# Performance work log

Hardware: AMD Instinct MI355X
Metric: run time of the kernel (lower is better)

Reference implementation:

```python
import jax, jax.numpy as jnp
import numpy as np

DIM = 640
HEADS = 8
SEG = DIM // 5                  # 128 per-segment channels
CH = (DIM // 5 * 4) // HEADS    # 64 per-head dim of the attention branch
SCALE = (DIM // HEADS) ** -0.5  # head_dim in __init__ uses full dim
EPS = 1e-5


def hardswish(x):
    return x * jnp.clip(x + 3.0, 0.0, 6.0) * (1.0 / 6.0)


def dwconv(x, w, pad):
    # x: (B,C,H,W), w: (C,kh,kw) depthwise kernel
    c = x.shape[1]
    return jax.lax.conv_general_dilated(
        x, w[:, None], (1, 1), [(pad, pad), (pad, pad)],
        feature_group_count=c, dimension_numbers=('NCHW', 'OIHW', 'NCHW'))


def pconv(x, w):
    # 1x1 pointwise conv, w: (out,in)
    return jnp.einsum('bchw,oc->bohw', x, w)


def bneval(x, g, b):
    # eval-mode BatchNorm2d with running_mean=0, running_var=1
    s = g * (1.0 / jnp.sqrt(1.0 + EPS))
    return x * s[None, :, None, None] + b[None, :, None, None]


def layernorm(x, g, b):
    m = x.mean(-1, keepdims=True)
    v = x.var(-1, keepdims=True)
    return (x - m) / jnp.sqrt(v + EPS) * g + b


def aggregator(x, Hs, Ws, dw3, dw5, dw7, pw, ln_g, ln_b, bn_g, bn_b):
    # x: (B_,N,C) -> heads tensor (B_,h,N,Ch) for 4 attention segments + local Agg_0 branch (B_,N,SEG)
    B_, N, C = x.shape
    xi = x.transpose(0, 2, 1).reshape(B_, C, Hs, Ws)
    segs = [xi[:, i * SEG:(i + 1) * SEG] for i in range(5)]
    # Agg_0: sepconv3x3 -> LayerNorm(channel-last) -> hardswish
    loc = pconv(dwconv(segs[4], dw3[0], 1), pw[0])
    loc = hardswish(layernorm(loc.reshape(B_, SEG, N).transpose(0, 2, 1), ln_g, ln_b))
    x0 = hardswish(bneval(segs[0], bn_g[0], bn_b[0]))
    x1 = hardswish(bneval(pconv(dwconv(segs[1], dw3[1], 1), pw[1]), bn_g[1], bn_b[1]))
    x2 = hardswish(bneval(pconv(dwconv(segs[2], dw5, 2), pw[2]), bn_g[2], bn_b[2]))
    x3 = hardswish(bneval(pconv(dwconv(segs[3], dw7, 3), pw[3]), bn_g[3], bn_b[3]))
    xt = jnp.concatenate([x0, x1, x2, x3], axis=1)           # (B_, 4*SEG, H, W)
    xt = xt.reshape(B_, HEADS, CH, N).transpose(0, 1, 3, 2)  # (B_, h, N, Ch)
    return xt, loc


def conv_rel_pos_enc(q, v, Hs, Ws, w3, w5, w7):
    # grouped depthwise convs over v image, head splits {3:2,5:3,7:3}
    B, h, N, Ch = q.shape
    v_img = v.transpose(0, 1, 3, 2).reshape(B, h * Ch, Hs, Ws)
    s1, s2 = 2 * Ch, 5 * Ch
    c = jnp.concatenate([dwconv(v_img[:, :s1], w3, 1),
                         dwconv(v_img[:, s1:s2], w5, 2),
                         dwconv(v_img[:, s2:], w7, 3)], axis=1)
    c = c.reshape(B, h, Ch, N).transpose(0, 1, 3, 2)
    return q * c


def _forward(x, y, kv_w, proj_w, proj_b, crpe_w3, crpe_w5, crpe_w7,
             aq_dw3, aq_dw5, aq_dw7, aq_pw, aq_ln_g, aq_ln_b, aq_bn_g, aq_bn_b,
             akv_dw3, akv_dw5, akv_dw7, akv_pw, akv_ln_g, akv_ln_b, akv_bn_g, akv_bn_b,
             Hs, Ws):
    B = x.shape[0]
    N = Hs * Ws
    kv = jnp.einsum('bhwc,oc->bhwo', x, kv_w).reshape(B, Hs, Ws, 2, DIM)
    kv = kv.transpose(3, 0, 1, 2, 4).reshape(2 * B, N, DIM)
    q = y.reshape(B, N, DIM)
    kvh, kv_loc = aggregator(kv, Hs, Ws, akv_dw3, akv_dw5, akv_dw7, akv_pw,
                             akv_ln_g, akv_ln_b, akv_bn_g, akv_bn_b)
    qh, q_loc = aggregator(q, Hs, Ws, aq_dw3, aq_dw5, aq_dw7, aq_pw,
                           aq_ln_g, aq_ln_b, aq_bn_g, aq_bn_b)
    kvh = kvh.reshape(2, B, HEADS, N, CH)
    k, v = kvh[0], kvh[1]
    kv_loc = kv_loc.reshape(2, B, N, SEG)[1]  # local features from the v branch
    k_sm = jax.nn.softmax(k, axis=2)                        # softmax over tokens
    kTv = jnp.einsum('bhnk,bhnv->bhkv', k_sm, v)            # (B,h,Ch,Ch)
    eff = jnp.einsum('bhnk,bhkv->bhnv', qh, kTv)            # (B,h,N,Ch)
    cr = conv_rel_pos_enc(qh, v, Hs, Ws, crpe_w3, crpe_w5, crpe_w7)
    o = SCALE * eff + cr
    o = o.transpose(0, 2, 1, 3).reshape(B, N, HEADS * CH)   # (B,N,4*SEG)
    o = jnp.concatenate([o, kv_loc + q_loc], axis=-1)       # (B,N,DIM)
    return jnp.einsum('bnc,oc->bno', o, proj_w) + proj_b


def setup_inputs():
    ks = jax.random.split(jax.random.key(0), 24)
    def n(i, shape, s=1.0):
        return jax.random.normal(ks[i], shape, dtype=jnp.float32) * s
    inp = {
        'x': n(0, (8, 64, 64, 640)), 'y': n(1, (8, 64, 64, 640)),
        'kv_w': n(2, (1280, 640), 0.02), 'proj_w': n(3, (640, 640), 0.02), 'proj_b': n(4, (640,), 0.02),
        'crpe_w3': n(5, (128, 3, 3), 0.1), 'crpe_w5': n(6, (192, 5, 5), 0.05), 'crpe_w7': n(7, (192, 7, 7), 0.03),
        'aq_dw3': n(8, (2, 128, 3, 3), 0.1), 'aq_dw5': n(9, (128, 5, 5), 0.05), 'aq_dw7': n(10, (128, 7, 7), 0.03),
        'aq_pw': n(11, (4, 128, 128), 0.05),
        'aq_ln_g': 1.0 + n(12, (128,), 0.1), 'aq_ln_b': n(13, (128,), 0.1),
        'aq_bn_g': 1.0 + n(14, (4, 128), 0.1), 'aq_bn_b': n(15, (4, 128), 0.1),
        'akv_dw3': n(16, (2, 128, 3, 3), 0.1), 'akv_dw5': n(17, (128, 5, 5), 0.05), 'akv_dw7': n(18, (128, 7, 7), 0.03),
        'akv_pw': n(19, (4, 128, 128), 0.05),
        'akv_ln_g': 1.0 + n(20, (128,), 0.1), 'akv_ln_b': n(21, (128,), 0.1),
        'akv_bn_g': 1.0 + n(22, (4, 128), 0.1), 'akv_bn_b': n(23, (4, 128), 0.1),
        'H': 64, 'W': 64,
    }
    return inp


def reference(x, y, kv_w, proj_w, proj_b, crpe_w3, crpe_w5, crpe_w7,
              aq_dw3, aq_dw5, aq_dw7, aq_pw, aq_ln_g, aq_ln_b, aq_bn_g, aq_bn_b,
              akv_dw3, akv_dw5, akv_dw7, akv_pw, akv_ln_g, akv_ln_b, akv_bn_g, akv_bn_b,
              H, W):
    return _forward(x, y, kv_w, proj_w, proj_b, crpe_w3, crpe_w5, crpe_w7,
                    aq_dw3, aq_dw5, aq_dw7, aq_pw, aq_ln_g, aq_ln_b, aq_bn_g, aq_bn_b,
                    akv_dw3, akv_dw5, akv_dw7, akv_pw, akv_ln_g, akv_ln_b, akv_bn_g, akv_bn_b,
                    H, W)
```

## Files before the change

### kernel.cpp

```cpp
#include <hip/hip_runtime.h>
#include <hip/hip_bf16.h>
#include <stdint.h>

#define BATCH 8
#define NTOK 4096
#define DIM 640
#define SEG 128
#define NHEADS 8
#define CH 64
#define SCALE_F 0.11180339887498948f
#define EPS_F 1e-5f
#define BNSCALE 0.99999500003749972f

typedef unsigned short u16;
typedef float f32x4 __attribute__((ext_vector_type(4)));
typedef short bf16x8 __attribute__((ext_vector_type(8)));

__device__ __forceinline__ float b2f(u16 u){
  union { float f; unsigned int i; } c; c.i = ((unsigned int)u)<<16; return c.f;
}
__device__ __forceinline__ u16 f2b(float f){
  union { float f; unsigned int i; } c; c.f = f;
  unsigned int i = c.i;
  return (u16)((i + 0x7fffu + ((i>>16)&1u)) >> 16);
}
__device__ __forceinline__ float hswish(float v){
  return v * fminf(fmaxf(v+3.f,0.f),6.f) * (1.f/6.f);
}

__global__ void cvt_k(const float* __restrict__ in, u16* __restrict__ out, int n){
  int idx = (blockIdx.x*256 + threadIdx.x)*4;
  if (idx>=n) return;
  float4 v = *(const float4*)(in+idx);
  ushort4 o;
  o.x=f2b(v.x); o.y=f2b(v.y); o.z=f2b(v.z); o.w=f2b(v.w);
  *(ushort4*)(out+idx) = o;
}

template<int MODE>
__global__ __launch_bounds__(256)
void mgemm(const u16* __restrict__ A, const u16* __restrict__ Wt,
           const float* __restrict__ e1, const float* __restrict__ e2,
           void* __restrict__ out, int K, int headbase)
{
  __shared__ u16 As[128*64];
  __shared__ u16 Bs[128*64];
  int tid = threadIdx.x;
  int wid = tid>>6, lane = tid&63;
  int rb = blockIdx.x*128, cb = blockIdx.y*128;
  int wr = wid>>1, wc = wid&1;
  f32x4 acc[4][4];
  #pragma unroll
  for (int m=0;m<4;m++)
    #pragma unroll
    for (int n=0;n<4;n++) acc[m][n] = (f32x4){0.f,0.f,0.f,0.f};

  const u16* Ab = A + (size_t)rb*K;
  const u16* Bb = Wt + (size_t)cb*K;
  int srow = wid*32 + (lane>>3);
  int scol = (lane&7)*8;

  for (int k0=0;k0<K;k0+=64){
    #pragma unroll
    for (int i=0;i<4;i++){
      const u16* sa = Ab + (size_t)(srow + i*8)*K + k0 + scol;
      const u16* sb = Bb + (size_t)(srow + i*8)*K + k0 + scol;
      u16* la = As + (wid*32 + i*8)*64;
      u16* lb = Bs + (wid*32 + i*8)*64;
      __builtin_amdgcn_global_load_lds((const __attribute__((address_space(1))) void*)sa,
                                       (__attribute__((address_space(3))) void*)la, 16, 0, 0);
      __builtin_amdgcn_global_load_lds((const __attribute__((address_space(1))) void*)sb,
                                       (__attribute__((address_space(3))) void*)lb, 16, 0, 0);
    }
    __syncthreads();
    int fr = lane&15, fk = (lane>>4)*8;
    #pragma unroll
    for (int kk=0;kk<64;kk+=32){
      bf16x8 af[4], bfr[4];
      #pragma unroll
      for (int m=0;m<4;m++) af[m] = *(const bf16x8*)&As[(wr*64 + m*16 + fr)*64 + kk + fk];
      #pragma unroll
      for (int n=0;n<4;n++) bfr[n] = *(const bf16x8*)&Bs[(wc*64 + n*16 + fr)*64 + kk + fk];
      #pragma unroll
      for (int m=0;m<4;m++)
        #pragma unroll
        for (int n=0;n<4;n++)
          acc[m][n] = __builtin_amdgcn_mfma_f32_16x16x32_bf16(af[m], bfr[n], acc[m][n], 0, 0, 0);
    }
    __syncthreads();
  }

  int fr = lane&15, fq = lane>>4;
  #pragma unroll
  for (int m=0;m<4;m++){
    #pragma unroll
    for (int j=0;j<4;j++){
      int r = rb + wr*64 + m*16 + fq*4 + j;
      int bb = r>>12, ntk = r&4095;
      #pragma unroll
      for (int n=0;n<4;n++){
        int o = cb + wc*64 + n*16 + fr;
        float v = acc[m][n][j];
        if (MODE==0){
          int s = (o>=DIM)?1:0; int co = o - s*DIM;
          ((u16*)out)[(((size_t)(s*BATCH+bb))*NTOK + ntk)*DIM + co] = f2b(v);
        } else if (MODE==1){
          ((float*)out)[(size_t)r*DIM + o] = v + e1[o];
        } else {
          float val = hswish(v * (e1[o]*BNSCALE) + e2[o]);
          int head = headbase + (o>>6), c = o&63;
          ((u16*)out)[(((size_t)bb*NHEADS + head)*NTOK + ntk)*CH + c] = f2b(val);
        }
      }
    }
  }
}

template<int T, bool INF32>
__global__ __launch_bounds__(256)
void conv_tile(const void* __restrict__ in, const float* __restrict__ w,
               u16* __restrict__ out, int NI2,
               size_t S1, size_t S2, int PXS,
               size_t SO1, size_t SO2, int OPXS)
{
  constexpr int P = T>>1;
  constexpr int PW = 15 + T;
  __shared__ u16 lds[PW*PW*64];
  int tid = threadIdx.x;
  int tile = blockIdx.x;
  int ty0 = (tile>>2)*16, tx0 = (tile&3)*16;
  int i = blockIdx.y;
  int i1 = i / NI2, i2 = i - i1*NI2;
  size_t in_off = (size_t)i1*S1 + (size_t)i2*S2;
  size_t out_off = (size_t)i1*SO1 + (size_t)i2*SO2;
  int c = tid & 63;

  float wreg[T*T];
  {
    const float* wp = w + (size_t)(i2*64 + c)*(T*T);
    #pragma unroll
    for (int j=0;j<T*T;j++) wreg[j] = wp[j];
  }

  if constexpr (!INF32){
    int l8 = tid&7;
    for (int p = tid>>3; p < PW*PW; p += 32){
      int py = p/PW, pxx = p - py*PW;
      int gy = ty0+py-P, gx = tx0+pxx-P;
      uint4 val = {0u,0u,0u,0u};
      if ((unsigned)gy<64u && (unsigned)gx<64u)
        val = *(const uint4*)((const u16*)in + in_off + (size_t)(gy*64+gx)*PXS + l8*8);
      *(uint4*)&lds[p*64 + l8*8] = val;
    }
  } else {
    int l16 = tid&15;
    for (int p = tid>>4; p < PW*PW; p += 16){
      int py = p/PW, pxx = p - py*PW;
      int gy = ty0+py-P, gx = tx0+pxx-P;
      ushort4 o4 = {0,0,0,0};
      if ((unsigned)gy<64u && (unsigned)gx<64u){
        float4 v = *(const float4*)((const float*)in + in_off + (size_t)(gy*64+gx)*PXS + l16*4);
        o4.x=f2b(v.x); o4.y=f2b(v.y); o4.z=f2b(v.z); o4.w=f2b(v.w);
      }
      *(ushort4*)&lds[p*64 + l16*4] = o4;
    }
  }
  __syncthreads();

  int ox0 = (tid>>6)*4;
  #pragma unroll 1
  for (int r=0;r<16;r++){
    float a0=0.f,a1=0.f,a2=0.f,a3=0.f;
    #pragma unroll
    for (int dy=0;dy<T;dy++){
      const u16* rowp = &lds[((r+dy)*PW + ox0)*64 + c];
      #pragma unroll
      for (int dxx=0;dxx<T+3;dxx++){
        float v = b2f(rowp[dxx*64]);
        if (dxx<T)             a0 += wreg[dy*T+dxx]*v;
        if (dxx>=1 && dxx<T+1) a1 += wreg[dy*T+dxx-1]*v;
        if (dxx>=2 && dxx<T+2) a2 += wreg[dy*T+dxx-2]*v;
        if (dxx>=3)            a3 += wreg[dy*T+dxx-3]*v;
      }
    }
    size_t ob = out_off + (size_t)((ty0+r)*64 + tx0+ox0)*OPXS + c;
    out[ob]          = f2b(a0);
    out[ob +   (size_t)OPXS] = f2b(a1);
    out[ob + 2*(size_t)OPXS] = f2b(a2);
    out[ob + 3*(size_t)OPXS] = f2b(a3);
  }
}

template<bool INF32>
__global__ void x0_k(const void* __restrict__ in, const float* __restrict__ g,
                     const float* __restrict__ b, u16* __restrict__ hout, int total)
{
  int idx = blockIdx.x*256 + threadIdx.x;
  if (idx>=total) return;
  int c = idx&127; int n = (idx>>7)&4095; int bb = idx>>19;
  size_t ofs = ((size_t)bb*NTOK+n)*DIM + c;
  float xv = INF32 ? ((const float*)in)[ofs] : b2f(((const u16*)in)[ofs]);
  float v = xv * (g[c]*BNSCALE) + b[c];
  v = hswish(v);
  int head = c>>6, ch = c&63;
  hout[(((size_t)bb*NHEADS+head)*NTOK+n)*CH+ch] = f2b(v);
}

__global__ __launch_bounds__(256)
void pconv_ln(const u16* __restrict__ A, const float* __restrict__ W,
              const float* __restrict__ g, const float* __restrict__ bp,
              u16* __restrict__ out)
{
  __shared__ float Wc[128][36];
  __shared__ float Ac[32][36];
  int tid = threadIdx.x;
  int r0 = blockIdx.x*32;
  int ty = tid>>5, tx = tid&31;
  float acc[4][4] = {};
  for (int k0=0;k0<128;k0+=32){
    {
      int row = tid>>1, kk = (tid&1)*16;
      const float* wr = W + (size_t)row*128 + k0 + kk;
      float4 a0=*(const float4*)wr, a1=*(const float4*)(wr+4);
      float4 a2=*(const float4*)(wr+8), a3=*(const float4*)(wr+12);
      Wc[row][kk+0]=a0.x; Wc[row][kk+1]=a0.y; Wc[row][kk+2]=a0.z; Wc[row][kk+3]=a0.w;
      Wc[row][kk+4]=a1.x; Wc[row][kk+5]=a1.y; Wc[row][kk+6]=a1.z; Wc[row][kk+7]=a1.w;
      Wc[row][kk+8]=a2.x; Wc[row][kk+9]=a2.y; Wc[row][kk+10]=a2.z; Wc[row][kk+11]=a2.w;
      Wc[row][kk+12]=a3.x; Wc[row][kk+13]=a3.y; Wc[row][kk+14]=a3.z; Wc[row][kk+15]=a3.w;
    }
    {
      int row = tid>>3, kk = (tid&7)*4;
      uint2 p = *(const uint2*)(A + (size_t)(r0+row)*128 + k0 + kk);
      Ac[row][kk+0]=b2f((u16)(p.x&0xffffu)); Ac[row][kk+1]=b2f((u16)(p.x>>16));
      Ac[row][kk+2]=b2f((u16)(p.y&0xffffu)); Ac[row][kk+3]=b2f((u16)(p.y>>16));
    }
    __syncthreads();
    #pragma unroll
    for (int kk=0;kk<32;kk+=4){
      float4 av[4], wv[4];
      #pragma unroll
      for (int i=0;i<4;i++) av[i] = *(const float4*)&Ac[ty*4+i][kk];
      #pragma unroll
      for (int j=0;j<4;j++) wv[j] = *(const float4*)&Wc[tx*4+j][kk];
      #pragma unroll
      for (int i=0;i<4;i++)
        #pragma unroll
        for (int j=0;j<4;j++)
          acc[i][j] += av[i].x*wv[j].x + av[i].y*wv[j].y + av[i].z*wv[j].z + av[i].w*wv[j].w;
    }
    __syncthreads();
  }
  #pragma unroll
  for (int i=0;i<4;i++){
    float s1=0.f,s2=0.f;
    #pragma unroll
    for (int j=0;j<4;j++){ s1+=acc[i][j]; s2+=acc[i][j]*acc[i][j]; }
    for (int m=1;m<32;m<<=1){ s1 += __shfl_xor(s1,m,32); s2 += __shfl_xor(s2,m,32); }
    float mean = s1*(1.f/128.f);
    float var = s2*(1.f/128.f) - mean*mean;
    float rstd = 1.f/sqrtf(var + EPS_F);
    int r = r0 + ty*4 + i; int bb = r>>12; int n = r&4095;
    #pragma unroll
    for (int j=0;j<4;j++){
      int c = tx*4+j;
      float val = (acc[i][j]-mean)*rstd*g[c] + bp[c];
      out[((size_t)bb*NTOK+n)*SEG + c] = f2b(hswish(val));
    }
  }
}

__global__ __launch_bounds__(256)
void softmax_p1(const u16* __restrict__ kh, float* __restrict__ pm, float* __restrict__ ps)
{
  __shared__ float lm[4][64];
  __shared__ float lsum[4][64];
  int chunk = blockIdx.x, bh = blockIdx.y;
  int tid = threadIdx.x;
  int ch = tid&63, sub = tid>>6;
  const u16* kp = kh + ((size_t)bh*NTOK + chunk*256 + sub*64)*CH + ch;
  float mx = -1e30f;
  for (int t=0;t<64;t++) mx = fmaxf(mx, b2f(kp[(size_t)t*CH]));
  float sm = 0.f;
  for (int t=0;t<64;t++) sm += expf(b2f(kp[(size_t)t*CH]) - mx);
  lm[sub][ch]=mx; lsum[sub][ch]=sm;
  __syncthreads();
  if (sub==0){
    float M = lm[0][ch];
    #pragma unroll
    for (int i=1;i<4;i++) M = fmaxf(M, lm[i][ch]);
    float S = 0.f;
    #pragma unroll
    for (int i=0;i<4;i++) S += lsum[i][ch]*expf(lm[i][ch]-M);
    pm[((size_t)bh*16+chunk)*64+ch]=M;
    ps[((size_t)bh*16+chunk)*64+ch]=S;
  }
}

__global__ void softmax_p2(const float* __restrict__ pm, const float* __restrict__ ps,
                           float* __restrict__ m, float* __restrict__ s)
{
  int bh = blockIdx.x, ch = threadIdx.x;
  float M = -1e30f;
  for (int c=0;c<16;c++) M = fmaxf(M, pm[((size_t)bh*16+c)*64+ch]);
  float S = 0.f;
  for (int c=0;c<16;c++) S += ps[((size_t)bh*16+c)*64+ch]*expf(pm[((size_t)bh*16+c)*64+ch]-M);
  m[bh*CH+ch]=M; s[bh*CH+ch]=S;
}

__global__ __launch_bounds__(256)
void ktv_partial(const u16* __restrict__ kh, const u16* __restrict__ vh,
                 const float* __restrict__ m, float* __restrict__ part)
{
  __shared__ float ek[8][64];
  __shared__ float vv[8][64];
  __shared__ float msh[64];
  int bh = blockIdx.y, chunk = blockIdx.x;
  int tid = threadIdx.x;
  const u16* kp = kh + ((size_t)bh*NTOK + chunk*256)*CH;
  const u16* vp = vh + ((size_t)bh*NTOK + chunk*256)*CH;
  if (tid<64) msh[tid]=m[bh*CH+tid];
  __syncthreads();
  int tkc = tid>>4, tvc = tid&15;
  float acc[4][4]={};
  for (int nn=0;nn<256;nn+=8){
    for (int e=tid;e<512;e+=256){
      int r=e>>6, c=e&63;
      ek[r][c]=expf(b2f(kp[(size_t)(nn+r)*CH+c]) - msh[c]);
      vv[r][c]=b2f(vp[(size_t)(nn+r)*CH+c]);
    }
    __syncthreads();
    #pragma unroll
    for (int i=0;i<8;i++){
      float a[4],b[4];
      #pragma unroll
      for(int u=0;u<4;u++) a[u]=ek[i][tkc*4+u];
      #pragma unroll
      for(int u=0;u<4;u++) b[u]=vv[i][tvc*4+u];
      #pragma unroll
      for(int u=0;u<4;u++)
        #pragma unroll
        for(int w=0;w<4;w++) acc[u][w]+=a[u]*b[w];
    }
    __syncthreads();
  }
  float* pp = part + (((size_t)bh*16 + chunk)*CH*CH);
  #pragma unroll
  for(int u=0;u<4;u++)
    #pragma unroll
    for(int w=0;w<4;w++)
      pp[(tkc*4+u)*CH + tvc*4+w] = acc[u][w];
}

__global__ void ktv_reduce(const float* __restrict__ part, const float* __restrict__ s,
                           float* __restrict__ ktv)
{
  int bh = blockIdx.x; int tid = threadIdx.x;
  for (int o=tid;o<CH*CH;o+=256){
    float sum=0.f;
    for (int c=0;c<16;c++) sum += part[(((size_t)bh*16+c)*CH*CH)+o];
    ktv[(size_t)bh*CH*CH+o] = sum / s[bh*CH + (o>>6)];
  }
}

__global__ __launch_bounds__(256)
void oassm_k(const u16* __restrict__ qh, const float* __restrict__ ktv,
             const u16* __restrict__ cbuf, u16* __restrict__ obuf)
{
  __shared__ float kt[64][65];
  __shared__ u16 qs[64][64];
  int bh = blockIdx.y; int b=bh>>3, h=bh&7;
  int n0 = blockIdx.x*64;
  int tid = threadIdx.x;
  const float* kp = ktv + (size_t)bh*CH*CH;
  for (int e=tid;e<4096;e+=256) kt[e>>6][e&63]=kp[e];
  const u16* qp = qh + ((size_t)bh*NTOK + n0)*CH;
  for (int e=tid;e<4096;e+=256) qs[e>>6][e&63]=qp[e];
  __syncthreads();
  int tn=tid>>4, tv=tid&15;
  float eff[4][4]={};
  for (int kc=0;kc<64;kc++){
    float a[4],w[4];
    #pragma unroll
    for(int i=0;i<4;i++) a[i]=b2f(qs[tn*4+i][kc]);
    #pragma unroll
    for(int j=0;j<4;j++) w[j]=kt[kc][tv*4+j];
    #pragma unroll
    for(int i=0;i<4;i++)
      #pragma unroll
      for(int j=0;j<4;j++) eff[i][j]+=a[i]*w[j];
  }
  #pragma unroll
  for (int i=0;i<4;i++){
    int n=n0+tn*4+i;
    const u16* cp = cbuf + ((size_t)bh*NTOK+n)*CH;
    u16* op = obuf + ((size_t)b*NTOK+n)*DIM + h*CH;
    #pragma unroll
    for (int j=0;j<4;j++){
      int vc=tv*4+j;
      float val = SCALE_F*eff[i][j] + b2f(qs[tn*4+i][vc])*b2f(cp[vc]);
      op[vc]=f2b(val);
    }
  }
}

__global__ void loccat_k(const u16* __restrict__ l1, const u16* __restrict__ l2,
                         u16* __restrict__ obuf)
{
  int idx = blockIdx.x*256+threadIdx.x;
  int j = idx&127; int n=(idx>>7)&4095; int bb=idx>>19;
  obuf[((size_t)bb*NTOK+n)*DIM + 512 + j] = f2b(b2f(l1[idx]) + b2f(l2[idx]));
}

extern "C" void kernel_launch(void* const* d_in, const int* in_sizes, int n_in,
                              void* d_out, int out_size, void* d_ws, size_t ws_size,
                              hipStream_t stream)
{
  const float* x = (const float*)d_in[0];
  const float* y = (const float*)d_in[1];
  const float* kv_w = (const float*)d_in[2];
  const float* proj_w = (const float*)d_in[3];
  const float* proj_b = (const float*)d_in[4];
  const float* crpe_w3 = (const float*)d_in[5];
  const float* crpe_w5 = (const float*)d_in[6];
  const float* crpe_w7 = (const float*)d_in[7];
  const float* aq_dw3 = (const float*)d_in[8];
  const float* aq_dw5 = (const float*)d_in[9];
  const float* aq_dw7 = (const float*)d_in[10];
  const float* aq_pw  = (const float*)d_in[11];
  const float* aq_ln_g = (const float*)d_in[12];
  const float* aq_ln_b = (const float*)d_in[13];
  const float* aq_bn_g = (const float*)d_in[14];
  const float* aq_bn_b = (const float*)d_in[15];
  const float* akv_dw3 = (const float*)d_in[16];
  const float* akv_dw5 = (const float*)d_in[17];
  const float* akv_dw7 = (const float*)d_in[18];
  const float* akv_pw  = (const float*)d_in[19];
  const float* akv_ln_g = (const float*)d_in[20];
  const float* akv_ln_b = (const float*)d_in[21];
  const float* akv_bn_g = (const float*)d_in[22];
  const float* akv_bn_b = (const float*)d_in[23];

  char* ws = (char*)d_ws;
  size_t off=0;
  auto alloc=[&](size_t bytes)->char*{ char* p = ws+off; off=(off+bytes+255)&~(size_t)255; return p; };
  u16* kvbuf = (u16*)alloc((size_t)16*NTOK*DIM*2);
  u16* kvh   = (u16*)alloc((size_t)16*NHEADS*NTOK*CH*2);
  u16* qh    = (u16*)alloc((size_t)8*NHEADS*NTOK*CH*2);
  u16* dwbuf = (u16*)alloc((size_t)16*NTOK*SEG*2);
  u16* kvloc = (u16*)alloc((size_t)8*NTOK*SEG*2);
  u16* qloc  = (u16*)alloc((size_t)8*NTOK*SEG*2);
  float* mbuf = (float*)alloc((size_t)64*64*4);
  float* sbuf = (float*)alloc((size_t)64*64*4);
  float* pmb  = (float*)alloc((size_t)64*16*64*4);
  float* psb  = (float*)alloc((size_t)64*16*64*4);
  float* part = (float*)alloc((size_t)64*16*64*64*4);
  float* ktv  = (float*)alloc((size_t)64*64*64*4);
  u16* cbuf  = (u16*)alloc((size_t)64*NTOK*CH*2);
  u16* xb    = (u16*)alloc((size_t)BATCH*NTOK*DIM*2);
  u16* kvwb  = (u16*)alloc((size_t)2*DIM*DIM*2);
  u16* pwb   = (u16*)alloc((size_t)DIM*DIM*2);
  u16* aqpwb = (u16*)alloc((size_t)4*SEG*SEG*2);
  u16* akvpwb= (u16*)alloc((size_t)4*SEG*SEG*2);
  u16* obuf  = kvbuf;

  const size_t SIMG = (size_t)NTOK*DIM;
  const size_t SDW  = (size_t)NTOK*SEG;
  const size_t SHD  = (size_t)NTOK*CH;

  {
    int nx = BATCH*NTOK*DIM;
    cvt_k<<<(nx/4+255)/256,256,0,stream>>>(x, xb, nx);
    int nw = 2*DIM*DIM;
    cvt_k<<<(nw/4+255)/256,256,0,stream>>>(kv_w, kvwb, nw);
    int np = DIM*DIM;
    cvt_k<<<(np/4+255)/256,256,0,stream>>>(proj_w, pwb, np);
    int na = 4*SEG*SEG;
    cvt_k<<<(na/4+255)/256,256,0,stream>>>(aq_pw, aqpwb, na);
    cvt_k<<<(na/4+255)/256,256,0,stream>>>(akv_pw, akvpwb, na);
  }

  mgemm<0><<<dim3(256,10),256,0,stream>>>(xb, kvwb, nullptr, nullptr, kvbuf, DIM, 0);

  {
    int tot = 16*NTOK*SEG;
    x0_k<false><<<tot/256,256,0,stream>>>(kvbuf, akv_bn_g, akv_bn_b, kvh, tot);
    conv_tile<3,false><<<dim3(16,32),256,0,stream>>>(kvbuf+128, akv_dw3+1152, dwbuf, 2, SIMG, 64, DIM, SDW, 64, SEG);
    mgemm<2><<<dim3(512,1),256,0,stream>>>(dwbuf, akvpwb+1*16384, akv_bn_g+128, akv_bn_b+128, kvh, 128, 2);
    conv_tile<5,false><<<dim3(16,32),256,0,stream>>>(kvbuf+256, akv_dw5, dwbuf, 2, SIMG, 64, DIM, SDW, 64, SEG);
    mgemm<2><<<dim3(512,1),256,0,stream>>>(dwbuf, akvpwb+2*16384, akv_bn_g+256, akv_bn_b+256, kvh, 128, 4);
    conv_tile<7,false><<<dim3(16,32),256,0,stream>>>(kvbuf+384, akv_dw7, dwbuf, 2, SIMG, 64, DIM, SDW, 64, SEG);
    mgemm<2><<<dim3(512,1),256,0,stream>>>(dwbuf, akvpwb+3*16384, akv_bn_g+384, akv_bn_b+384, kvh, 128, 6);
    conv_tile<3,false><<<dim3(16,16),256,0,stream>>>(kvbuf + (size_t)8*SIMG + 512, akv_dw3, dwbuf, 2, SIMG, 64, DIM, SDW, 64, SEG);
    pconv_ln<<<8*NTOK/32,256,0,stream>>>(dwbuf, akv_pw, akv_ln_g, akv_ln_b, kvloc);
  }
  {
    int tot = 8*NTOK*SEG;
    x0_k<true><<<tot/256,256,0,stream>>>(y, aq_bn_g, aq_bn_b, qh, tot);
    conv_tile<3,true><<<dim3(16,16),256,0,stream>>>(y+128, aq_dw3+1152, dwbuf, 2, SIMG, 64, DIM, SDW, 64, SEG);
    mgemm<2><<<dim3(256,1),256,0,stream>>>(dwbuf, aqpwb+1*16384, aq_bn_g+128, aq_bn_b+128, qh, 128, 2);
    conv_tile<5,true><<<dim3(16,16),256,0,stream>>>(y+256, aq_dw5, dwbuf, 2, SIMG, 64, DIM, SDW, 64, SEG);
    mgemm<2><<<dim3(256,1),256,0,stream>>>(dwbuf, aqpwb+2*16384, aq_bn_g+256, aq_bn_b+256, qh, 128, 4);
    conv_tile<7,true><<<dim3(16,16),256,0,stream>>>(y+384, aq_dw7, dwbuf, 2, SIMG, 64, DIM, SDW, 64, SEG);
    mgemm<2><<<dim3(256,1),256,0,stream>>>(dwbuf, aqpwb+3*16384, aq_bn_g+384, aq_bn_b+384, qh, 128, 6);
    conv_tile<3,true><<<dim3(16,16),256,0,stream>>>(y+512, aq_dw3, dwbuf, 2, SIMG, 64, DIM, SDW, 64, SEG);
    pconv_ln<<<8*NTOK/32,256,0,stream>>>(dwbuf, aq_pw, aq_ln_g, aq_ln_b, qloc);
  }
  const u16* vh = kvh + (size_t)8*NHEADS*NTOK*CH;
  softmax_p1<<<dim3(16,64),256,0,stream>>>(kvh, pmb, psb);
  softmax_p2<<<64,64,0,stream>>>(pmb, psb, mbuf, sbuf);
  ktv_partial<<<dim3(16,64),256,0,stream>>>(kvh, vh, mbuf, part);
  ktv_reduce<<<64,256,0,stream>>>(part, sbuf, ktv);
  conv_tile<3,false><<<dim3(16,16),256,0,stream>>>(vh, crpe_w3, cbuf, 2, 8*SHD, SHD, CH, 8*SHD, SHD, CH);
  conv_tile<5,false><<<dim3(16,24),256,0,stream>>>(vh + 2*SHD, crpe_w5, cbuf + 2*SHD, 3, 8*SHD, SHD, CH, 8*SHD, SHD, CH);
  conv_tile<7,false><<<dim3(16,24),256,0,stream>>>(vh + 5*SHD, crpe_w7, cbuf + 5*SHD, 3, 8*SHD, SHD, CH, 8*SHD, SHD, CH);
  oassm_k<<<dim3(64,64),256,0,stream>>>(qh, ktv, cbuf, obuf);
  loccat_k<<<8*NTOK*SEG/256,256,0,stream>>>(kvloc, qloc, obuf);
  mgemm<1><<<dim3(256,5),256,0,stream>>>(obuf, pwb, proj_b, nullptr, (float*)d_out, DIM, 0);
}
```

Before: 910.4 us.

## Fuse branch kernels, batch pointwise GEMMs, MFMA output assembly, and swizzled block order

Several changes land together. The four weight conversions are merged into one kernel, and the x0 BN/hardswish for the kv path is fused into the kv GEMM epilogue. The three per-segment pointwise GEMMs are batched into one launch over separate conv buffers, and the local-branch sum is fused into the second pconv_ln so loccat is no longer needed. The q·ktv output assembly is rewritten to use bf16 MFMA with a transposed bf16 ktv, ktv partials are halved, and block indices are swizzled. The aim is to cut launch count and memory traffic, at the cost of aliasing workspace buffers and rounding ktv to bf16.

```diff
diff --git a/kernel.cpp b/kernel.cpp
--- a/kernel.cpp
+++ b/kernel.cpp
@@ -27,6 +27,9 @@
 __device__ __forceinline__ float hswish(float v){
   return v * fminf(fmaxf(v+3.f,0.f),6.f) * (1.f/6.f);
 }
+__device__ __forceinline__ int swz(int bx, int n){
+  return (bx&7)*(n>>3) + (bx>>3);
+}
 
 __global__ void cvt_k(const float* __restrict__ in, u16* __restrict__ out, int n){
   int idx = (blockIdx.x*256 + threadIdx.x)*4;
@@ -37,17 +40,47 @@
   *(ushort4*)(out+idx) = o;
 }
 
+__global__ void cvtw_k(const float* __restrict__ w0, const float* __restrict__ w1,
+                       const float* __restrict__ w2, const float* __restrict__ w3,
+                       u16* __restrict__ o0, u16* __restrict__ o1,
+                       u16* __restrict__ o2, u16* __restrict__ o3){
+  int i4 = blockIdx.x*256 + threadIdx.x;
+  const int n0=819200/4, n1=409600/4, n2=65536/4, n3=65536/4;
+  const float* src; u16* dst; int idx;
+  if (i4 < n0){ src=w0; dst=o0; idx=i4; }
+  else if (i4 < n0+n1){ src=w1; dst=o1; idx=i4-n0; }
+  else if (i4 < n0+n1+n2){ src=w2; dst=o2; idx=i4-n0-n1; }
+  else if (i4 < n0+n1+n2+n3){ src=w3; dst=o3; idx=i4-n0-n1-n2; }
+  else return;
+  float4 v = *(const float4*)(src + (size_t)idx*4);
+  ushort4 o; o.x=f2b(v.x); o.y=f2b(v.y); o.z=f2b(v.z); o.w=f2b(v.w);
+  *(ushort4*)(dst + (size_t)idx*4) = o;
+}
+
 template<int MODE>
 __global__ __launch_bounds__(256)
 void mgemm(const u16* __restrict__ A, const u16* __restrict__ Wt,
            const float* __restrict__ e1, const float* __restrict__ e2,
-           void* __restrict__ out, int K, int headbase)
+           void* __restrict__ out, int K, int headbase, size_t abr,
+           const float* __restrict__ bng, const float* __restrict__ bnb,
+           u16* __restrict__ hout)
 {
   __shared__ u16 As[128*64];
   __shared__ u16 Bs[128*64];
   int tid = threadIdx.x;
   int wid = tid>>6, lane = tid&63;
-  int rb = blockIdx.x*128, cb = blockIdx.y*128;
+  int bx = swz(blockIdx.x, gridDim.x);
+  int rb = bx*128, cb;
+  if (MODE==2){
+    int br = blockIdx.y;
+    A  += (size_t)br*abr;
+    Wt += (size_t)br*16384;
+    e1 += br*128; e2 += br*128;
+    headbase += 2*br;
+    cb = 0;
+  } else {
+    cb = blockIdx.y*128;
+  }
   int wr = wid>>1, wc = wid&1;
   f32x4 acc[4][4];
   #pragma unroll
@@ -104,6 +137,11 @@
         if (MODE==0){
           int s = (o>=DIM)?1:0; int co = o - s*DIM;
           ((u16*)out)[(((size_t)(s*BATCH+bb))*NTOK + ntk)*DIM + co] = f2b(v);
+          if (co < 128){
+            float hv = hswish(v*(bng[co]*BNSCALE) + bnb[co]);
+            int img = s*BATCH + bb;
+            hout[(((size_t)img*NHEADS + (co>>6))*NTOK + ntk)*CH + (co&63)] = f2b(hv);
+          }
         } else if (MODE==1){
           ((float*)out)[(size_t)r*DIM + o] = v + e1[o];
         } else {
@@ -184,32 +222,31 @@
       }
     }
     size_t ob = out_off + (size_t)((ty0+r)*64 + tx0+ox0)*OPXS + c;
-    out[ob]          = f2b(a0);
+    out[ob]                  = f2b(a0);
     out[ob +   (size_t)OPXS] = f2b(a1);
     out[ob + 2*(size_t)OPXS] = f2b(a2);
     out[ob + 3*(size_t)OPXS] = f2b(a3);
   }
 }
 
-template<bool INF32>
-__global__ void x0_k(const void* __restrict__ in, const float* __restrict__ g,
+__global__ void x0_k(const float* __restrict__ in, const float* __restrict__ g,
                      const float* __restrict__ b, u16* __restrict__ hout, int total)
 {
   int idx = blockIdx.x*256 + threadIdx.x;
   if (idx>=total) return;
   int c = idx&127; int n = (idx>>7)&4095; int bb = idx>>19;
-  size_t ofs = ((size_t)bb*NTOK+n)*DIM + c;
-  float xv = INF32 ? ((const float*)in)[ofs] : b2f(((const u16*)in)[ofs]);
-  float v = xv * (g[c]*BNSCALE) + b[c];
-  v = hswish(v);
+  float xv = in[((size_t)bb*NTOK+n)*DIM + c];
+  float v = hswish(xv * (g[c]*BNSCALE) + b[c]);
   int head = c>>6, ch = c&63;
   hout[(((size_t)bb*NHEADS+head)*NTOK+n)*CH+ch] = f2b(v);
 }
 
+template<bool ADD>
 __global__ __launch_bounds__(256)
 void pconv_ln(const u16* __restrict__ A, const float* __restrict__ W,
               const float* __restrict__ g, const float* __restrict__ bp,
-              u16* __restrict__ out)
+              u16* __restrict__ out, int ostr, int obase,
+              const u16* __restrict__ addsrc)
 {
   __shared__ float Wc[128][36];
   __shared__ float Ac[32][36];
@@ -263,8 +300,9 @@
     #pragma unroll
     for (int j=0;j<4;j++){
       int c = tx*4+j;
-      float val = (acc[i][j]-mean)*rstd*g[c] + bp[c];
-      out[((size_t)bb*NTOK+n)*SEG + c] = f2b(hswish(val));
+      float val = hswish((acc[i][j]-mean)*rstd*g[c] + bp[c]);
+      if (ADD) val += b2f(addsrc[((size_t)bb*NTOK+n)*SEG + c]);
+      out[((size_t)bb*NTOK+n)*ostr + obase + c] = f2b(val);
     }
   }
 }
@@ -316,13 +354,13 @@
   __shared__ float msh[64];
   int bh = blockIdx.y, chunk = blockIdx.x;
   int tid = threadIdx.x;
-  const u16* kp = kh + ((size_t)bh*NTOK + chunk*256)*CH;
-  const u16* vp = vh + ((size_t)bh*NTOK + chunk*256)*CH;
+  const u16* kp = kh + ((size_t)bh*NTOK + chunk*512)*CH;
+  const u16* vp = vh + ((size_t)bh*NTOK + chunk*512)*CH;
   if (tid<64) msh[tid]=m[bh*CH+tid];
   __syncthreads();
   int tkc = tid>>4, tvc = tid&15;
   float acc[4][4]={};
-  for (int nn=0;nn<256;nn+=8){
+  for (int nn=0;nn<512;nn+=8){
     for (int e=tid;e<512;e+=256){
       int r=e>>6, c=e&63;
       ek[r][c]=expf(b2f(kp[(size_t)(nn+r)*CH+c]) - msh[c]);
@@ -343,7 +381,7 @@
     }
     __syncthreads();
   }
-  float* pp = part + (((size_t)bh*16 + chunk)*CH*CH);
+  float* pp = part + (((size_t)bh*8 + chunk)*CH*CH);
   #pragma unroll
   for(int u=0;u<4;u++)
     #pragma unroll
@@ -352,63 +390,84 @@
 }
 
 __global__ void ktv_reduce(const float* __restrict__ part, const float* __restrict__ s,
-                           float* __restrict__ ktv)
+                           u16* __restrict__ ktvT)
 {
   int bh = blockIdx.x; int tid = threadIdx.x;
   for (int o=tid;o<CH*CH;o+=256){
     float sum=0.f;
-    for (int c=0;c<16;c++) sum += part[(((size_t)bh*16+c)*CH*CH)+o];
-    ktv[(size_t)bh*CH*CH+o] = sum / s[bh*CH + (o>>6)];
+    for (int c=0;c<8;c++) sum += part[(((size_t)bh*8+c)*CH*CH)+o];
+    int kc = o>>6, vc = o&63;
+    ktvT[(size_t)bh*CH*CH + vc*CH + kc] = f2b(sum / s[bh*CH + kc]);
   }
 }
 
 __global__ __launch_bounds__(256)
-void oassm_k(const u16* __restrict__ qh, const float* __restrict__ ktv,
-             const u16* __restrict__ cbuf, u16* __restrict__ obuf)
-{
-  __shared__ float kt[64][65];
-  __shared__ u16 qs[64][64];
-  int bh = blockIdx.y; int b=bh>>3, h=bh&7;
-  int n0 = blockIdx.x*64;
+void oeff_k(const u16* __restrict__ qh, const u16* __restrict__ ktvT,
+            const u16* __restrict__ cbuf, u16* __restrict__ obuf)
+{
+  __shared__ u16 qs[128*64];
+  __shared__ u16 kt[64*64];
   int tid = threadIdx.x;
-  const float* kp = ktv + (size_t)bh*CH*CH;
-  for (int e=tid;e<4096;e+=256) kt[e>>6][e&63]=kp[e];
+  int wid = tid>>6, lane = tid&63;
+  int bx = swz(blockIdx.x, gridDim.x);
+  int bh = blockIdx.y; int b = bh>>3, h = bh&7;
+  int n0 = bx*128;
   const u16* qp = qh + ((size_t)bh*NTOK + n0)*CH;
-  for (int e=tid;e<4096;e+=256) qs[e>>6][e&63]=qp[e];
+  const u16* kp = ktvT + (size_t)bh*CH*CH;
+  int srow = lane>>3, scol = (lane&7)*8;
+  #pragma unroll
+  for (int i=0;i<4;i++){
+    const u16* sa = qp + (size_t)(wid*32 + i*8 + srow)*CH + scol;
+    u16* la = qs + (wid*32 + i*8)*64;
+    __builtin_amdgcn_global_load_lds((const __attribute__((address_space(1))) void*)sa,
+                                     (__attribute__((address_space(3))) void*)la, 16, 0, 0);
+  }
+  #pragma unroll
+  for (int i=0;i<2;i++){
+    const u16* sb = kp + (size_t)(wid*16 + i*8 + srow)*CH + scol;
+    u16* lb = kt + (wid*16 + i*8)*64;
+    __builtin_amdgcn_global_load_lds((const __attribute__((address_space(1))) void*)sb,
+                                     (__attribute__((address_space(3))) void*)lb, 16, 0, 0);
+  }
   __syncthreads();
-  int tn=tid>>4, tv=tid&15;
-  float eff[4][4]={};
-  for (int kc=0;kc<64;kc++){
-    float a[4],w[4];
-    #pragma unroll
-    for(int i=0;i<4;i++) a[i]=b2f(qs[tn*4+i][kc]);
-    #pragma unroll
-    for(int j=0;j<4;j++) w[j]=kt[kc][tv*4+j];
-    #pragma unroll
-    for(int i=0;i<4;i++)
-      #pragma unroll
-      for(int j=0;j<4;j++) eff[i][j]+=a[i]*w[j];
-  }
-  #pragma unroll
-  for (int i=0;i<4;i++){
-    int n=n0+tn*4+i;
-    const u16* cp = cbuf + ((size_t)bh*NTOK+n)*CH;
-    u16* op = obuf + ((size_t)b*NTOK+n)*DIM + h*CH;
+
+  int fr = lane&15, fk = (lane>>4)*8;
+  f32x4 acc[2][4];
+  #pragma unroll
+  for (int m=0;m<2;m++)
+    #pragma unroll
+    for (int n=0;n<4;n++) acc[m][n] = (f32x4){0.f,0.f,0.f,0.f};
+  #pragma unroll
+  for (int kk=0;kk<64;kk+=32){
+    bf16x8 af[2], bfr[4];
+    #pragma unroll
+    for (int m=0;m<2;m++) af[m] = *(const bf16x8*)&qs[(wid*32 + m*16 + fr)*64 + kk + fk];
+    #pragma unroll
+    for (int n=0;n<4;n++) bfr[n] = *(const bf16x8*)&kt[(n*16 + fr)*64 + kk + fk];
+    #pragma unroll
+    for (int m=0;m<2;m++)
+      #pragma unroll
+      for (int n=0;n<4;n++)
+        acc[m][n] = __builtin_amdgcn_mfma_f32_16x16x32_bf16(af[m], bfr[n], acc[m][n], 0, 0, 0);
+  }
+
+  int fq = lane>>4;
+  #pragma unroll
+  for (int m=0;m<2;m++){
     #pragma unroll
     for (int j=0;j<4;j++){
-      int vc=tv*4+j;
-      float val = SCALE_F*eff[i][j] + b2f(qs[tn*4+i][vc])*b2f(cp[vc]);
-      op[vc]=f2b(val);
-    }
-  }
-}
-
-__global__ void loccat_k(const u16* __restrict__ l1, const u16* __restrict__ l2,
-                         u16* __restrict__ obuf)
-{
-  int idx = blockIdx.x*256+threadIdx.x;
-  int j = idx&127; int n=(idx>>7)&4095; int bb=idx>>19;
-  obuf[((size_t)bb*NTOK+n)*DIM + 512 + j] = f2b(b2f(l1[idx]) + b2f(l2[idx]));
+      int rl = wid*32 + m*16 + fq*4 + j;
+      int tok = n0 + rl;
+      const u16* cp = cbuf + ((size_t)bh*NTOK + tok)*CH;
+      u16* op = obuf + ((size_t)b*NTOK + tok)*DIM + h*CH;
+      #pragma unroll
+      for (int n=0;n<4;n++){
+        int col = n*16 + fr;
+        float val = SCALE_F*acc[m][n][j] + b2f(qs[rl*64 + col])*b2f(cp[col]);
+        op[col] = f2b(val);
+      }
+    }
+  }
 }
 
 extern "C" void kernel_launch(void* const* d_in, const int* in_sizes, int n_in,
@@ -440,80 +499,73 @@
   const float* akv_bn_g = (const float*)d_in[22];
   const float* akv_bn_b = (const float*)d_in[23];
 
+  const size_t SIMG = (size_t)NTOK*DIM;
+  const size_t SDW  = (size_t)NTOK*SEG;
+  const size_t SHD  = (size_t)NTOK*CH;
+
   char* ws = (char*)d_ws;
   size_t off=0;
   auto alloc=[&](size_t bytes)->char*{ char* p = ws+off; off=(off+bytes+255)&~(size_t)255; return p; };
-  u16* kvbuf = (u16*)alloc((size_t)16*NTOK*DIM*2);
-  u16* kvh   = (u16*)alloc((size_t)16*NHEADS*NTOK*CH*2);
-  u16* qh    = (u16*)alloc((size_t)8*NHEADS*NTOK*CH*2);
-  u16* dwbuf = (u16*)alloc((size_t)16*NTOK*SEG*2);
-  u16* kvloc = (u16*)alloc((size_t)8*NTOK*SEG*2);
-  u16* qloc  = (u16*)alloc((size_t)8*NTOK*SEG*2);
+  u16* kvbuf = (u16*)alloc((size_t)16*SIMG*2);
+  u16* kvh   = (u16*)alloc((size_t)16*NHEADS*SHD*2);
+  u16* qh    = (u16*)alloc((size_t)8*NHEADS*SHD*2);
+  char* dwbR = alloc((size_t)3*16*SDW*2);
+  u16* dwb0  = (u16*)dwbR;
+  u16* dwb1  = dwb0 + (size_t)16*SDW;
+  u16* dwb2  = dwb1 + (size_t)16*SDW;
+  float* part = (float*)dwbR;
+  u16* ktvT  = (u16*)(dwbR + 8*1024*1024 + 512*1024);
+  u16* cbuf  = (u16*)(dwbR + 10*1024*1024);
+  u16* kvloc = (u16*)alloc((size_t)8*SDW*2);
   float* mbuf = (float*)alloc((size_t)64*64*4);
   float* sbuf = (float*)alloc((size_t)64*64*4);
   float* pmb  = (float*)alloc((size_t)64*16*64*4);
   float* psb  = (float*)alloc((size_t)64*16*64*4);
-  float* part = (float*)alloc((size_t)64*16*64*64*4);
-  float* ktv  = (float*)alloc((size_t)64*64*64*4);
-  u16* cbuf  = (u16*)alloc((size_t)64*NTOK*CH*2);
-  u16* xb    = (u16*)alloc((size_t)BATCH*NTOK*DIM*2);
+  u16* xb    = (u16*)alloc((size_t)BATCH*SIMG*2);
   u16* kvwb  = (u16*)alloc((size_t)2*DIM*DIM*2);
   u16* pwb   = (u16*)alloc((size_t)DIM*DIM*2);
   u16* aqpwb = (u16*)alloc((size_t)4*SEG*SEG*2);
   u16* akvpwb= (u16*)alloc((size_t)4*SEG*SEG*2);
   u16* obuf  = kvbuf;
 
-  const size_t SIMG = (size_t)NTOK*DIM;
-  const size_t SDW  = (size_t)NTOK*SEG;
-  const size_t SHD  = (size_t)NTOK*CH;
-
   {
     int nx = BATCH*NTOK*DIM;
     cvt_k<<<(nx/4+255)/256,256,0,stream>>>(x, xb, nx);
-    int nw = 2*DIM*DIM;
-    cvt_k<<<(nw/4+255)/256,256,0,stream>>>(kv_w, kvwb, nw);
-    int np = DIM*DIM;
-    cvt_k<<<(np/4+255)/256,256,0,stream>>>(proj_w, pwb, np);
-    int na = 4*SEG*SEG;
-    cvt_k<<<(na/4+255)/256,256,0,stream>>>(aq_pw, aqpwb, na);
-    cvt_k<<<(na/4+255)/256,256,0,stream>>>(akv_pw, akvpwb, na);
-  }
-
-  mgemm<0><<<dim3(256,10),256,0,stream>>>(xb, kvwb, nullptr, nullptr, kvbuf, DIM, 0);
+    cvtw_k<<<1329,256,0,stream>>>(kv_w, proj_w, aq_pw, akv_pw, kvwb, pwb, aqpwb, akvpwb);
+  }
+
+  mgemm<0><<<dim3(256,10),256,0,stream>>>(xb, kvwb, nullptr, nullptr, kvbuf, DIM, 0, 0,
+                                          akv_bn_g, akv_bn_b, kvh);
 
   {
-    int tot = 16*NTOK*SEG;
-    x0_k<false><<<tot/256,256,0,stream>>>(kvbuf, akv_bn_g, akv_bn_b, kvh, tot);
-    conv_tile<3,false><<<dim3(16,32),256,0,stream>>>(kvbuf+128, akv_dw3+1152, dwbuf, 2, SIMG, 64, DIM, SDW, 64, SEG);
-    mgemm<2><<<dim3(512,1),256,0,stream>>>(dwbuf, akvpwb+1*16384, akv_bn_g+128, akv_bn_b+128, kvh, 128, 2);
-    conv_tile<5,false><<<dim3(16,32),256,0,stream>>>(kvbuf+256, akv_dw5, dwbuf, 2, SIMG, 64, DIM, SDW, 64, SEG);
-    mgemm<2><<<dim3(512,1),256,0,stream>>>(dwbuf, akvpwb+2*16384, akv_bn_g+256, akv_bn_b+256, kvh, 128, 4);
-    conv_tile<7,false><<<dim3(16,32),256,0,stream>>>(kvbuf+384, akv_dw7, dwbuf, 2, SIMG, 64, DIM, SDW, 64, SEG);
-    mgemm<2><<<dim3(512,1),256,0,stream>>>(dwbuf, akvpwb+3*16384, akv_bn_g+384, akv_bn_b+384, kvh, 128, 6);
-    conv_tile<3,false><<<dim3(16,16),256,0,stream>>>(kvbuf + (size_t)8*SIMG + 512, akv_dw3, dwbuf, 2, SIMG, 64, DIM, SDW, 64, SEG);
-    pconv_ln<<<8*NTOK/32,256,0,stream>>>(dwbuf, akv_pw, akv_ln_g, akv_ln_b, kvloc);
+    conv_tile<3,false><<<dim3(16,32),256,0,stream>>>(kvbuf+128, akv_dw3+1152, dwb0, 2, SIMG, 64, DIM, SDW, 64, SEG);
+    conv_tile<5,false><<<dim3(16,32),256,0,stream>>>(kvbuf+256, akv_dw5,      dwb1, 2, SIMG, 64, DIM, SDW, 64, SEG);
+    conv_tile<7,false><<<dim3(16,32),256,0,stream>>>(kvbuf+384, akv_dw7,      dwb2, 2, SIMG, 64, DIM, SDW, 64, SEG);
+    mgemm<2><<<dim3(512,3),256,0,stream>>>(dwb0, akvpwb+16384, akv_bn_g+128, akv_bn_b+128, kvh, 128, 2,
+                                           (size_t)16*SDW, nullptr, nullptr, nullptr);
+    conv_tile<3,false><<<dim3(16,16),256,0,stream>>>(kvbuf + (size_t)8*SIMG + 512, akv_dw3, dwb0, 2, SIMG, 64, DIM, SDW, 64, SEG);
+    pconv_ln<false><<<8*NTOK/32,256,0,stream>>>(dwb0, akv_pw, akv_ln_g, akv_ln_b, kvloc, SEG, 0, nullptr);
   }
   {
     int tot = 8*NTOK*SEG;
-    x0_k<true><<<tot/256,256,0,stream>>>(y, aq_bn_g, aq_bn_b, qh, tot);
-    conv_tile<3,true><<<dim3(16,16),256,0,stream>>>(y+128, aq_dw3+1152, dwbuf, 2, SIMG, 64, DIM, SDW, 64, SEG);
-    mgemm<2><<<dim3(256,1),256,0,stream>>>(dwbuf, aqpwb+1*16384, aq_bn_g+128, aq_bn_b+128, qh, 128, 2);
-    conv_tile<5,true><<<dim3(16,16),256,0,stream>>>(y+256, aq_dw5, dwbuf, 2, SIMG, 64, DIM, SDW, 64, SEG);
-    mgemm<2><<<dim3(256,1),256,0,stream>>>(dwbuf, aqpwb+2*16384, aq_bn_g+256, aq_bn_b+256, qh, 128, 4);
-    conv_tile<7,true><<<dim3(16,16),256,0,stream>>>(y+384, aq_dw7, dwbuf, 2, SIMG, 64, DIM, SDW, 64, SEG);
-    mgemm<2><<<dim3(256,1),256,0,stream>>>(dwbuf, aqpwb+3*16384, aq_bn_g+384, aq_bn_b+384, qh, 128, 6);
-    conv_tile<3,true><<<dim3(16,16),256,0,stream>>>(y+512, aq_dw3, dwbuf, 2, SIMG, 64, DIM, SDW, 64, SEG);
-    pconv_ln<<<8*NTOK/32,256,0,stream>>>(dwbuf, aq_pw, aq_ln_g, aq_ln_b, qloc);
-  }
-  const u16* vh = kvh + (size_t)8*NHEADS*NTOK*CH;
+    x0_k<<<tot/256,256,0,stream>>>(y, aq_bn_g, aq_bn_b, qh, tot);
+    conv_tile<3,true><<<dim3(16,16),256,0,stream>>>(y+128, aq_dw3+1152, dwb0, 2, SIMG, 64, DIM, SDW, 64, SEG);
+    conv_tile<5,true><<<dim3(16,16),256,0,stream>>>(y+256, aq_dw5,      dwb1, 2, SIMG, 64, DIM, SDW, 64, SEG);
+    conv_tile<7,true><<<dim3(16,16),256,0,stream>>>(y+384, aq_dw7,      dwb2, 2, SIMG, 64, DIM, SDW, 64, SEG);
+    mgemm<2><<<dim3(256,3),256,0,stream>>>(dwb0, aqpwb+16384, aq_bn_g+128, aq_bn_b+128, qh, 128, 2,
+                                           (size_t)16*SDW, nullptr, nullptr, nullptr);
+    conv_tile<3,true><<<dim3(16,16),256,0,stream>>>(y+512, aq_dw3, dwb0, 2, SIMG, 64, DIM, SDW, 64, SEG);
+    pconv_ln<true><<<8*NTOK/32,256,0,stream>>>(dwb0, aq_pw, aq_ln_g, aq_ln_b, obuf, DIM, 512, kvloc);
+  }
+  const u16* vh = kvh + (size_t)8*NHEADS*SHD;
   softmax_p1<<<dim3(16,64),256,0,stream>>>(kvh, pmb, psb);
   softmax_p2<<<64,64,0,stream>>>(pmb, psb, mbuf, sbuf);
-  ktv_partial<<<dim3(16,64),256,0,stream>>>(kvh, vh, mbuf, part);
-  ktv_reduce<<<64,256,0,stream>>>(part, sbuf, ktv);
-  conv_tile<3,false><<<dim3(16,16),256,0,stream>>>(vh, crpe_w3, cbuf, 2, 8*SHD, SHD, CH, 8*SHD, SHD, CH);
+  ktv_partial<<<dim3(8,64),256,0,stream>>>(kvh, vh, mbuf, part);
+  ktv_reduce<<<64,256,0,stream>>>(part, sbuf, ktvT);
+  conv_tile<3,false><<<dim3(16,16),256,0,stream>>>(vh,         crpe_w3, cbuf,         2, 8*SHD, SHD, CH, 8*SHD, SHD, CH);
   conv_tile<5,false><<<dim3(16,24),256,0,stream>>>(vh + 2*SHD, crpe_w5, cbuf + 2*SHD, 3, 8*SHD, SHD, CH, 8*SHD, SHD, CH);
   conv_tile<7,false><<<dim3(16,24),256,0,stream>>>(vh + 5*SHD, crpe_w7, cbuf + 5*SHD, 3, 8*SHD, SHD, CH, 8*SHD, SHD, CH);
-  oassm_k<<<dim3(64,64),256,0,stream>>>(qh, ktv, cbuf, obuf);
-  loccat_k<<<8*NTOK*SEG/256,256,0,stream>>>(kvloc, qloc, obuf);
-  mgemm<1><<<dim3(256,5),256,0,stream>>>(obuf, pwb, proj_b, nullptr, (float*)d_out, DIM, 0);
-}
+  oeff_k<<<dim3(32,64),256,0,stream>>>(qh, ktvT, cbuf, obuf);
+  mgemm<1><<<dim3(256,5),256,0,stream>>>(obuf, pwb, proj_b, nullptr, (float*)d_out, DIM, 0, 0,
+                                         nullptr, nullptr, nullptr);
+}
```

After: 900.6 us. About the same (-1.1%).
